# Kernel tuning notes

Hardware: AMD Instinct MI355X
Metric: run time of the kernel (lower is better)

## Reference

```python
import jax, jax.numpy as jnp
import numpy as np

B, T, S = 4, 64, 256
E_ENC = 512   # encoder_hidden_size
D_DEC = 512   # decoder_hidden_size (must equal E_ENC per original math)
F_EMB = 128   # field_embed_size


def setup_inputs() -> dict:
    key = jax.random.key(0)
    ks = jax.random.split(key, 11)
    s = 0.05
    return {
        "output": jax.random.normal(ks[0], (B, T, D_DEC), jnp.float32),
        "encoder_hidden": jax.random.normal(ks[1], (S, B, E_ENC), jnp.float32),
        "input_z": jax.random.normal(ks[2], (B, S, F_EMB), jnp.float32),
        "W1": jax.random.normal(ks[3], (D_DEC, E_ENC), jnp.float32) * s,
        "b1": jnp.zeros((D_DEC,), jnp.float32),
        "W2": jax.random.normal(ks[4], (D_DEC, D_DEC), jnp.float32) * s,
        "b2": jnp.zeros((D_DEC,), jnp.float32),
        "W3": jax.random.normal(ks[5], (D_DEC, F_EMB), jnp.float32) * s,
        "b3": jnp.zeros((D_DEC,), jnp.float32),
        "W4": jax.random.normal(ks[6], (D_DEC, D_DEC), jnp.float32) * s,
        "b4": jnp.zeros((D_DEC,), jnp.float32),
    }


def reference(output, encoder_hidden, input_z, W1, b1, W2, b2, W3, b3, W4, b4):
    # out_hs: tanh(lin1(encoder_hidden)) on [S,B,D], then .view -> reshape to [B,S,D]
    out_hs = jnp.tanh(jnp.einsum('sbe,de->sbd', encoder_hidden, W1) + b1)
    out_hs = out_hs.reshape(out_hs.shape[1], out_hs.shape[0], out_hs.shape[2])  # [B,S,D] (raw view, as in torch)
    enc_r = encoder_hidden.reshape(encoder_hidden.shape[1], encoder_hidden.shape[0], encoder_hidden.shape[2])  # [B,S,E]

    out_fds = jnp.tanh(jnp.einsum('bsf,df->bsd', input_z, W3) + b3)   # [B,S,D]
    out2 = jnp.tanh(jnp.einsum('btd,ed->bte', output, W2) + b2)       # [B,T,D]
    out3 = jnp.tanh(jnp.einsum('btd,ed->bte', output, W4) + b4)       # [B,T,D]

    # Multiplicative gates, vectorized over decoder timesteps t: [B,T,S,D]
    g1 = out_hs[:, None, :, :] * out2[:, :, None, :]
    alpha = jax.nn.softmax(g1, axis=2)   # softmax over encoder positions S
    g2 = out_fds[:, None, :, :] * out3[:, :, None, :]
    beta = jax.nn.softmax(g2, axis=2)

    q = alpha * beta
    qn = jax.lax.stop_gradient(jnp.sum(q, axis=2, keepdims=True))  # .detach() in torch
    gamma = q / qn

    attn = jnp.sum(gamma * enc_r[:, None, :, :], axis=2)           # [B,T,D]
    concat = jnp.concatenate([output, attn], axis=-1)              # [B,T,2D]
    return concat, attn
```

## Files before the change

kernel.cpp:

```cpp
#include <hip/hip_runtime.h>

#define BB 4
#define TT 64
#define SS 256
#define DD 512
#define FEMB 128

__device__ __forceinline__ float fast_tanh(float x) {
    x = fminf(fmaxf(x, -10.f), 10.f);
    float t = __expf(2.f * x);
    return (t - 1.f) / (t + 1.f);
}

__global__ __launch_bounds__(256) void gemm_tanh_kernel(
    const float* __restrict__ X, const float* __restrict__ Z, const float* __restrict__ Y,
    const float* __restrict__ W1, const float* __restrict__ b1,
    const float* __restrict__ W2, const float* __restrict__ b2,
    const float* __restrict__ W3, const float* __restrict__ b3,
    const float* __restrict__ W4, const float* __restrict__ b4,
    float* __restrict__ H, float* __restrict__ Fo,
    float* __restrict__ O2, float* __restrict__ O3)
{
    int id = blockIdx.x;
    const float* A; const float* W; const float* bias; float* C; int K;
    if (id < 128)      { A = X; W = W1; bias = b1; C = H;  K = 512; }
    else if (id < 256) { id -= 128; A = Z; W = W3; bias = b3; C = Fo; K = 128; }
    else if (id < 288) { id -= 256; A = Y; W = W2; bias = b2; C = O2; K = 512; }
    else               { id -= 288; A = Y; W = W4; bias = b4; C = O3; K = 512; }
    const int m0 = (id >> 3) * 64;
    const int n0 = (id & 7) * 64;

    __shared__ float As[16][68];
    __shared__ float Ws[16][68];

    const int tid  = threadIdx.x;
    const int lrow = tid >> 2;
    const int lkv  = tid & 3;
    const int ty   = tid >> 4;
    const int tx   = tid & 15;

    float acc[4][4] = {};

    const float* Ap = &A[(m0 + lrow) * K + lkv * 4];
    const float* Wp = &W[(n0 + lrow) * K + lkv * 4];
    float4 av = *(const float4*)Ap;
    float4 wv = *(const float4*)Wp;

    for (int k0 = 0; k0 < K; k0 += 16) {
        __syncthreads();
        As[lkv*4+0][lrow] = av.x; As[lkv*4+1][lrow] = av.y;
        As[lkv*4+2][lrow] = av.z; As[lkv*4+3][lrow] = av.w;
        Ws[lkv*4+0][lrow] = wv.x; Ws[lkv*4+1][lrow] = wv.y;
        Ws[lkv*4+2][lrow] = wv.z; Ws[lkv*4+3][lrow] = wv.w;
        __syncthreads();
        if (k0 + 16 < K) {
            av = *(const float4*)(Ap + k0 + 16);
            wv = *(const float4*)(Wp + k0 + 16);
        }
        #pragma unroll
        for (int k = 0; k < 16; ++k) {
            float4 a4 = *(const float4*)&As[k][ty * 4];
            float4 w4 = *(const float4*)&Ws[k][tx * 4];
            float a[4] = {a4.x, a4.y, a4.z, a4.w};
            float w[4] = {w4.x, w4.y, w4.z, w4.w};
            #pragma unroll
            for (int i = 0; i < 4; ++i)
                #pragma unroll
                for (int j = 0; j < 4; ++j)
                    acc[i][j] = fmaf(a[i], w[j], acc[i][j]);
        }
    }

    float4 bb = *(const float4*)&bias[n0 + tx * 4];
    float bj[4] = {bb.x, bb.y, bb.z, bb.w};
    #pragma unroll
    for (int i = 0; i < 4; ++i) {
        const int m = m0 + ty * 4 + i;
        float4 o;
        o.x = fast_tanh(acc[i][0] + bj[0]);
        o.y = fast_tanh(acc[i][1] + bj[1]);
        o.z = fast_tanh(acc[i][2] + bj[2]);
        o.w = fast_tanh(acc[i][3] + bj[3]);
        *(float4*)&C[m * DD + n0 + tx * 4] = o;
    }
}

__global__ __launch_bounds__(512) void attn_kernel(
    const float* __restrict__ H, const float* __restrict__ Fo,
    const float* __restrict__ X,
    const float* __restrict__ O2, const float* __restrict__ O3,
    const float* __restrict__ Y,
    float* __restrict__ out)
{
    const int idx = blockIdx.x;
    const int b   = (idx & 7) >> 1;
    const int rem = ((idx >> 3) << 1) | (idx & 1);
    const int t0  = (rem >> 2) * 2;
    const int dq  = rem & 3;
    const int tid = threadIdx.x;
    const int dl  = tid & 127;
    const int d   = dq * 128 + dl;
    const int sq  = tid >> 7;

    const int bt0 = b * TT + t0;
    const float u0 = O2[bt0 * DD + d],       v0 = O3[bt0 * DD + d];
    const float u1 = O2[(bt0 + 1) * DD + d], v1 = O3[(bt0 + 1) * DD + d];

    float l0 = 0.f, l1 = 0.f, a0 = 0.f, a1 = 0.f;
    const int base = (b * SS + sq * 64) * DD + d;
    const float* Hb = H  + base;
    const float* Fb = Fo + base;
    const float* Eb = X  + base;

    for (int s0 = 0; s0 < 64; s0 += 8) {
        float h[8], f[8], e[8];
        #pragma unroll
        for (int s = 0; s < 8; ++s) h[s] = Hb[(s0 + s) * DD];
        #pragma unroll
        for (int s = 0; s < 8; ++s) f[s] = Fb[(s0 + s) * DD];
        #pragma unroll
        for (int s = 0; s < 8; ++s) e[s] = Eb[(s0 + s) * DD];
        #pragma unroll
        for (int s = 0; s < 8; ++s) {
            const float w0 = fmaf(h[s], u0, f[s] * v0);
            const float x0 = __expf(w0);
            l0 += x0; a0 = fmaf(x0, e[s], a0);
            const float w1 = fmaf(h[s], u1, f[s] * v1);
            const float x1 = __expf(w1);
            l1 += x1; a1 = fmaf(x1, e[s], a1);
        }
    }

    __shared__ float red[3][128][9];
    if (sq) {
        red[sq-1][dl][0] = l0; red[sq-1][dl][1] = l1;
        red[sq-1][dl][2] = a0; red[sq-1][dl][3] = a1;
    }
    __syncthreads();
    if (sq == 0) {
        #pragma unroll
        for (int q = 0; q < 3; ++q) {
            l0 += red[q][dl][0]; l1 += red[q][dl][1];
            a0 += red[q][dl][2]; a1 += red[q][dl][3];
        }
        const float r0 = a0 / l0, r1 = a1 / l1;
        out[BB * TT * 2 * DD + bt0 * DD + d]       = r0;
        out[BB * TT * 2 * DD + (bt0 + 1) * DD + d] = r1;
        out[bt0 * 2 * DD + DD + d]                 = r0;
        out[(bt0 + 1) * 2 * DD + DD + d]           = r1;
        out[bt0 * 2 * DD + d]                      = Y[bt0 * DD + d];
        out[(bt0 + 1) * 2 * DD + d]                = Y[(bt0 + 1) * DD + d];
    }
}

extern "C" void kernel_launch(void* const* d_in, const int* in_sizes, int n_in,
                              void* d_out, int out_size, void* d_ws, size_t ws_size,
                              hipStream_t stream)
{
    const float* Y  = (const float*)d_in[0];
    const float* X  = (const float*)d_in[1];
    const float* Z  = (const float*)d_in[2];
    const float* W1 = (const float*)d_in[3];
    const float* b1 = (const float*)d_in[4];
    const float* W2 = (const float*)d_in[5];
    const float* b2 = (const float*)d_in[6];
    const float* W3 = (const float*)d_in[7];
    const float* b3 = (const float*)d_in[8];
    const float* W4 = (const float*)d_in[9];
    const float* b4 = (const float*)d_in[10];
    float* out = (float*)d_out;

    float* H  = (float*)d_ws;
    float* Fo = H  + 1024 * 512;
    float* O2 = Fo + 1024 * 512;
    float* O3 = O2 + 256 * 512;

    gemm_tanh_kernel<<<320, 256, 0, stream>>>(X, Z, Y, W1, b1, W2, b2, W3, b3, W4, b4,
                                              H, Fo, O2, O3);
    attn_kernel<<<512, 512, 0, stream>>>(H, Fo, X, O2, O3, Y, out);
}
```

Before: 118.1 us.

## Use bf16 MFMA for the four projection GEMMs with a conversion pre-pass

Adds a kernel that converts the activations and weights to bf16 in workspace. The FP32 LDS-tiled SIMT GEMM is replaced by a kernel that feeds matrix-core 16x16x32 bf16 instructions directly from global memory, with register double-buffering and no shared memory. The aim is to cut the compute time of the GEMM stage. In exchange it adds a kernel launch and extra memory traffic for the conversion, and it lowers input precision to bf16, which could push tolerance-sensitive outputs such as the exponentials in the attention kernel out of range.

```diff
diff --git a/kernel.cpp b/kernel.cpp
--- a/kernel.cpp
+++ b/kernel.cpp
@@ -6,82 +6,109 @@
 #define DD 512
 #define FEMB 128
 
+typedef __attribute__((ext_vector_type(8))) short short8;
+typedef __attribute__((ext_vector_type(4))) float floatx4;
+
 __device__ __forceinline__ float fast_tanh(float x) {
     x = fminf(fmaxf(x, -10.f), 10.f);
     float t = __expf(2.f * x);
     return (t - 1.f) / (t + 1.f);
 }
 
-__global__ __launch_bounds__(256) void gemm_tanh_kernel(
+__device__ __forceinline__ unsigned int pack_bf2(float a, float b) {
+    union { float f; unsigned int u; } ca, cb;
+    ca.f = a; cb.f = b;
+    unsigned int ua = ca.u + 0x7FFF + ((ca.u >> 16) & 1);
+    unsigned int ub = cb.u + 0x7FFF + ((cb.u >> 16) & 1);
+    return (ua >> 16) | (ub & 0xFFFF0000u);
+}
+
+__global__ __launch_bounds__(256) void cvt_kernel(
     const float* __restrict__ X, const float* __restrict__ Z, const float* __restrict__ Y,
-    const float* __restrict__ W1, const float* __restrict__ b1,
-    const float* __restrict__ W2, const float* __restrict__ b2,
-    const float* __restrict__ W3, const float* __restrict__ b3,
-    const float* __restrict__ W4, const float* __restrict__ b4,
+    const float* __restrict__ W1, const float* __restrict__ W2,
+    const float* __restrict__ W3, const float* __restrict__ W4,
+    unsigned short* __restrict__ Xb, unsigned short* __restrict__ Zb,
+    unsigned short* __restrict__ Yb, unsigned short* __restrict__ W1b,
+    unsigned short* __restrict__ W2b, unsigned short* __restrict__ W3b,
+    unsigned short* __restrict__ W4b)
+{
+    const int e = (blockIdx.x * 256 + threadIdx.x) * 4;
+    const float* src; unsigned short* dst; int off;
+    if (e < 524288)       { src = X;  dst = Xb;  off = 0; }
+    else if (e < 655360)  { src = Z;  dst = Zb;  off = 524288; }
+    else if (e < 786432)  { src = Y;  dst = Yb;  off = 655360; }
+    else if (e < 1048576) { src = W1; dst = W1b; off = 786432; }
+    else if (e < 1310720) { src = W2; dst = W2b; off = 1048576; }
+    else if (e < 1376256) { src = W3; dst = W3b; off = 1310720; }
+    else                  { src = W4; dst = W4b; off = 1376256; }
+    const int i = e - off;
+    float4 v = *(const float4*)&src[i];
+    uint2 p;
+    p.x = pack_bf2(v.x, v.y);
+    p.y = pack_bf2(v.z, v.w);
+    *(uint2*)&dst[i] = p;
+}
+
+__global__ __launch_bounds__(256) void gemm_mfma_kernel(
+    const unsigned short* __restrict__ Xb, const unsigned short* __restrict__ Zb,
+    const unsigned short* __restrict__ Yb,
+    const unsigned short* __restrict__ W1b, const unsigned short* __restrict__ W2b,
+    const unsigned short* __restrict__ W3b, const unsigned short* __restrict__ W4b,
+    const float* __restrict__ b1, const float* __restrict__ b2,
+    const float* __restrict__ b3, const float* __restrict__ b4,
     float* __restrict__ H, float* __restrict__ Fo,
     float* __restrict__ O2, float* __restrict__ O3)
 {
     int id = blockIdx.x;
-    const float* A; const float* W; const float* bias; float* C; int K;
-    if (id < 128)      { A = X; W = W1; bias = b1; C = H;  K = 512; }
-    else if (id < 256) { id -= 128; A = Z; W = W3; bias = b3; C = Fo; K = 128; }
-    else if (id < 288) { id -= 256; A = Y; W = W2; bias = b2; C = O2; K = 512; }
-    else               { id -= 288; A = Y; W = W4; bias = b4; C = O3; K = 512; }
+    const unsigned short* A; const unsigned short* W; const float* bias; float* C; int K;
+    if (id < 128)      { A = Xb; W = W1b; bias = b1; C = H;  K = 512; }
+    else if (id < 256) { id -= 128; A = Zb; W = W3b; bias = b3; C = Fo; K = 128; }
+    else if (id < 288) { id -= 256; A = Yb; W = W2b; bias = b2; C = O2; K = 512; }
+    else               { id -= 288; A = Yb; W = W4b; bias = b4; C = O3; K = 512; }
     const int m0 = (id >> 3) * 64;
     const int n0 = (id & 7) * 64;
-
-    __shared__ float As[16][68];
-    __shared__ float Ws[16][68];
-
-    const int tid  = threadIdx.x;
-    const int lrow = tid >> 2;
-    const int lkv  = tid & 3;
-    const int ty   = tid >> 4;
-    const int tx   = tid & 15;
-
-    float acc[4][4] = {};
-
-    const float* Ap = &A[(m0 + lrow) * K + lkv * 4];
-    const float* Wp = &W[(n0 + lrow) * K + lkv * 4];
-    float4 av = *(const float4*)Ap;
-    float4 wv = *(const float4*)Wp;
-
-    for (int k0 = 0; k0 < K; k0 += 16) {
-        __syncthreads();
-        As[lkv*4+0][lrow] = av.x; As[lkv*4+1][lrow] = av.y;
-        As[lkv*4+2][lrow] = av.z; As[lkv*4+3][lrow] = av.w;
-        Ws[lkv*4+0][lrow] = wv.x; Ws[lkv*4+1][lrow] = wv.y;
-        Ws[lkv*4+2][lrow] = wv.z; Ws[lkv*4+3][lrow] = wv.w;
-        __syncthreads();
-        if (k0 + 16 < K) {
-            av = *(const float4*)(Ap + k0 + 16);
-            wv = *(const float4*)(Wp + k0 + 16);
-        }
-        #pragma unroll
-        for (int k = 0; k < 16; ++k) {
-            float4 a4 = *(const float4*)&As[k][ty * 4];
-            float4 w4 = *(const float4*)&Ws[k][tx * 4];
-            float a[4] = {a4.x, a4.y, a4.z, a4.w};
-            float w[4] = {w4.x, w4.y, w4.z, w4.w};
-            #pragma unroll
-            for (int i = 0; i < 4; ++i)
-                #pragma unroll
-                for (int j = 0; j < 4; ++j)
-                    acc[i][j] = fmaf(a[i], w[j], acc[i][j]);
-        }
-    }
-
-    float4 bb = *(const float4*)&bias[n0 + tx * 4];
-    float bj[4] = {bb.x, bb.y, bb.z, bb.w};
+    const int wv   = threadIdx.x >> 6;
+    const int lane = threadIdx.x & 63;
+    const int fr   = lane & 15;
+    const int kh   = (lane >> 4) * 8;
+
+    const unsigned short* Ap = A + (m0 + wv * 16 + fr) * K + kh;
+    const unsigned short* Wp = W + (n0 + fr) * K + kh;
+    const int WS = 16 * K;
+
+    floatx4 acc0 = {0.f,0.f,0.f,0.f}, acc1 = acc0, acc2 = acc0, acc3 = acc0;
+
+    short8 a  = *(const short8*)Ap;
+    short8 w0 = *(const short8*)(Wp);
+    short8 w1 = *(const short8*)(Wp + WS);
+    short8 w2 = *(const short8*)(Wp + 2 * WS);
+    short8 w3 = *(const short8*)(Wp + 3 * WS);
+
+    for (int k0 = 0; k0 < K; k0 += 32) {
+        const int kn = (k0 + 32 < K) ? (k0 + 32) : 0;
+        short8 an  = *(const short8*)(Ap + kn);
+        short8 wn0 = *(const short8*)(Wp + kn);
+        short8 wn1 = *(const short8*)(Wp + WS + kn);
+        short8 wn2 = *(const short8*)(Wp + 2 * WS + kn);
+        short8 wn3 = *(const short8*)(Wp + 3 * WS + kn);
+        acc0 = __builtin_amdgcn_mfma_f32_16x16x32_bf16(a, w0, acc0, 0, 0, 0);
+        acc1 = __builtin_amdgcn_mfma_f32_16x16x32_bf16(a, w1, acc1, 0, 0, 0);
+        acc2 = __builtin_amdgcn_mfma_f32_16x16x32_bf16(a, w2, acc2, 0, 0, 0);
+        acc3 = __builtin_amdgcn_mfma_f32_16x16x32_bf16(a, w3, acc3, 0, 0, 0);
+        a = an; w0 = wn0; w1 = wn1; w2 = wn2; w3 = wn3;
+    }
+
+    const int orow  = m0 + wv * 16 + (lane >> 4) * 4;
+    const int ocol0 = n0 + fr;
+    const float bv0 = bias[ocol0], bv1 = bias[ocol0 + 16],
+                bv2 = bias[ocol0 + 32], bv3 = bias[ocol0 + 48];
     #pragma unroll
-    for (int i = 0; i < 4; ++i) {
-        const int m = m0 + ty * 4 + i;
-        float4 o;
-        o.x = fast_tanh(acc[i][0] + bj[0]);
-        o.y = fast_tanh(acc[i][1] + bj[1]);
-        o.z = fast_tanh(acc[i][2] + bj[2]);
-        o.w = fast_tanh(acc[i][3] + bj[3]);
-        *(float4*)&C[m * DD + n0 + tx * 4] = o;
+    for (int r = 0; r < 4; ++r) {
+        float* Cr = C + (orow + r) * DD + ocol0;
+        Cr[0]  = fast_tanh(acc0[r] + bv0);
+        Cr[16] = fast_tanh(acc1[r] + bv1);
+        Cr[32] = fast_tanh(acc2[r] + bv2);
+        Cr[48] = fast_tanh(acc3[r] + bv3);
     }
 }
 
@@ -174,8 +201,17 @@
     float* Fo = H  + 1024 * 512;
     float* O2 = Fo + 1024 * 512;
     float* O3 = O2 + 256 * 512;
-
-    gemm_tanh_kernel<<<320, 256, 0, stream>>>(X, Z, Y, W1, b1, W2, b2, W3, b3, W4, b4,
-                                              H, Fo, O2, O3);
+    unsigned short* Xb  = (unsigned short*)(O3 + 256 * 512);
+    unsigned short* Zb  = Xb  + 524288;
+    unsigned short* Yb  = Zb  + 131072;
+    unsigned short* W1b = Yb  + 131072;
+    unsigned short* W2b = W1b + 262144;
+    unsigned short* W3b = W2b + 262144;
+    unsigned short* W4b = W3b + 65536;
+
+    cvt_kernel<<<1600, 256, 0, stream>>>(X, Z, Y, W1, W2, W3, W4,
+                                         Xb, Zb, Yb, W1b, W2b, W3b, W4b);
+    gemm_mfma_kernel<<<320, 256, 0, stream>>>(Xb, Zb, Yb, W1b, W2b, W3b, W4b,
+                                              b1, b2, b3, b4, H, Fo, O2, O3);
     attn_kernel<<<512, 512, 0, stream>>>(H, Fo, X, O2, O3, Y, out);
 }
```

New measurement: 111.9 us. 1.06x faster.

## Replace FP32 shared-memory GEMM with bf16 MFMA loading operands straight from global

Applied to the files above, without the earlier changes.

The fused four-way linear+tanh GEMM now runs on MFMA 16x16x32 bf16 instructions. Each fp32 operand is truncated to bf16 with a byte permute, and fragments are loaded directly from global memory into registers with one-step prefetch, so the LDS staging and barriers are gone. This targets the scalar FMA cost of the GEMM stage. In exchange it loses precision through bf16 truncation, which feeds an exponent in the attention softmax, and it uses uncoalesced strided global loads with no LDS reuse.

```diff
diff --git a/kernel.cpp b/kernel.cpp
--- a/kernel.cpp
+++ b/kernel.cpp
@@ -6,13 +6,35 @@
 #define DD 512
 #define FEMB 128
 
+typedef __attribute__((ext_vector_type(8))) short short8;
+typedef __attribute__((ext_vector_type(4))) float floatx4;
+
 __device__ __forceinline__ float fast_tanh(float x) {
     x = fminf(fmaxf(x, -10.f), 10.f);
     float t = __expf(2.f * x);
     return (t - 1.f) / (t + 1.f);
 }
 
-__global__ __launch_bounds__(256) void gemm_tanh_kernel(
+struct f8 { float4 lo, hi; };
+__device__ __forceinline__ f8 ldf8(const float* p) {
+    f8 r;
+    r.lo = *(const float4*)p;
+    r.hi = *(const float4*)(p + 4);
+    return r;
+}
+__device__ __forceinline__ unsigned int fbits(float x) {
+    union { float f; unsigned int u; } c; c.f = x; return c.u;
+}
+__device__ __forceinline__ short8 cvt8(f8 v) {
+    union { unsigned int u[4]; short8 s; } r;
+    r.u[0] = __builtin_amdgcn_perm(fbits(v.lo.y), fbits(v.lo.x), 0x07060302u);
+    r.u[1] = __builtin_amdgcn_perm(fbits(v.lo.w), fbits(v.lo.z), 0x07060302u);
+    r.u[2] = __builtin_amdgcn_perm(fbits(v.hi.y), fbits(v.hi.x), 0x07060302u);
+    r.u[3] = __builtin_amdgcn_perm(fbits(v.hi.w), fbits(v.hi.z), 0x07060302u);
+    return r.s;
+}
+
+__global__ __launch_bounds__(256) void gemm_mfma_kernel(
     const float* __restrict__ X, const float* __restrict__ Z, const float* __restrict__ Y,
     const float* __restrict__ W1, const float* __restrict__ b1,
     const float* __restrict__ W2, const float* __restrict__ b2,
@@ -29,59 +51,53 @@
     else               { id -= 288; A = Y; W = W4; bias = b4; C = O3; K = 512; }
     const int m0 = (id >> 3) * 64;
     const int n0 = (id & 7) * 64;
+    const int wv   = threadIdx.x >> 6;
+    const int lane = threadIdx.x & 63;
+    const int fr   = lane & 15;
+    const int kh   = (lane >> 4) * 8;
 
-    __shared__ float As[16][68];
-    __shared__ float Ws[16][68];
+    const float* Ap = A + (m0 + wv * 16 + fr) * K + kh;
+    const float* Wp = W + (n0 + fr) * K + kh;
+    const int WS = 16 * K;
 
-    const int tid  = threadIdx.x;
-    const int lrow = tid >> 2;
-    const int lkv  = tid & 3;
-    const int ty   = tid >> 4;
-    const int tx   = tid & 15;
+    floatx4 acc0 = {0.f,0.f,0.f,0.f}, acc1 = acc0, acc2 = acc0, acc3 = acc0;
 
-    float acc[4][4] = {};
+    f8 ra  = ldf8(Ap);
+    f8 rw0 = ldf8(Wp);
+    f8 rw1 = ldf8(Wp + WS);
+    f8 rw2 = ldf8(Wp + 2 * WS);
+    f8 rw3 = ldf8(Wp + 3 * WS);
 
-    const float* Ap = &A[(m0 + lrow) * K + lkv * 4];
-    const float* Wp = &W[(n0 + lrow) * K + lkv * 4];
-    float4 av = *(const float4*)Ap;
-    float4 wv = *(const float4*)Wp;
-
-    for (int k0 = 0; k0 < K; k0 += 16) {
-        __syncthreads();
-        As[lkv*4+0][lrow] = av.x; As[lkv*4+1][lrow] = av.y;
-        As[lkv*4+2][lrow] = av.z; As[lkv*4+3][lrow] = av.w;
-        Ws[lkv*4+0][lrow] = wv.x; Ws[lkv*4+1][lrow] = wv.y;
-        Ws[lkv*4+2][lrow] = wv.z; Ws[lkv*4+3][lrow] = wv.w;
-        __syncthreads();
-        if (k0 + 16 < K) {
-            av = *(const float4*)(Ap + k0 + 16);
-            wv = *(const float4*)(Wp + k0 + 16);
-        }
-        #pragma unroll
-        for (int k = 0; k < 16; ++k) {
-            float4 a4 = *(const float4*)&As[k][ty * 4];
-            float4 w4 = *(const float4*)&Ws[k][tx * 4];
-            float a[4] = {a4.x, a4.y, a4.z, a4.w};
-            float w[4] = {w4.x, w4.y, w4.z, w4.w};
-            #pragma unroll
-            for (int i = 0; i < 4; ++i)
-                #pragma unroll
-                for (int j = 0; j < 4; ++j)
-                    acc[i][j] = fmaf(a[i], w[j], acc[i][j]);
-        }
+    for (int k0 = 0; k0 < K; k0 += 32) {
+        const int kn = (k0 + 32 < K) ? (k0 + 32) : 0;
+        f8 na  = ldf8(Ap + kn);
+        f8 nw0 = ldf8(Wp + kn);
+        f8 nw1 = ldf8(Wp + WS + kn);
+        f8 nw2 = ldf8(Wp + 2 * WS + kn);
+        f8 nw3 = ldf8(Wp + 3 * WS + kn);
+        short8 a  = cvt8(ra);
+        short8 w0 = cvt8(rw0);
+        short8 w1 = cvt8(rw1);
+        short8 w2 = cvt8(rw2);
+        short8 w3 = cvt8(rw3);
+        acc0 = __builtin_amdgcn_mfma_f32_16x16x32_bf16(a, w0, acc0, 0, 0, 0);
+        acc1 = __builtin_amdgcn_mfma_f32_16x16x32_bf16(a, w1, acc1, 0, 0, 0);
+        acc2 = __builtin_amdgcn_mfma_f32_16x16x32_bf16(a, w2, acc2, 0, 0, 0);
+        acc3 = __builtin_amdgcn_mfma_f32_16x16x32_bf16(a, w3, acc3, 0, 0, 0);
+        ra = na; rw0 = nw0; rw1 = nw1; rw2 = nw2; rw3 = nw3;
     }
 
-    float4 bb = *(const float4*)&bias[n0 + tx * 4];
-    float bj[4] = {bb.x, bb.y, bb.z, bb.w};
+    const int orow  = m0 + wv * 16 + (lane >> 4) * 4;
+    const int ocol0 = n0 + fr;
+    const float bv0 = bias[ocol0], bv1 = bias[ocol0 + 16],
+                bv2 = bias[ocol0 + 32], bv3 = bias[ocol0 + 48];
     #pragma unroll
-    for (int i = 0; i < 4; ++i) {
-        const int m = m0 + ty * 4 + i;
-        float4 o;
-        o.x = fast_tanh(acc[i][0] + bj[0]);
-        o.y = fast_tanh(acc[i][1] + bj[1]);
-        o.z = fast_tanh(acc[i][2] + bj[2]);
-        o.w = fast_tanh(acc[i][3] + bj[3]);
-        *(float4*)&C[m * DD + n0 + tx * 4] = o;
+    for (int r = 0; r < 4; ++r) {
+        float* Cr = C + (orow + r) * DD + ocol0;
+        Cr[0]  = fast_tanh(acc0[r] + bv0);
+        Cr[16] = fast_tanh(acc1[r] + bv1);
+        Cr[32] = fast_tanh(acc2[r] + bv2);
+        Cr[48] = fast_tanh(acc3[r] + bv3);
     }
 }
 
@@ -175,7 +191,7 @@
     float* O2 = Fo + 1024 * 512;
     float* O3 = O2 + 256 * 512;
 
-    gemm_tanh_kernel<<<320, 256, 0, stream>>>(X, Z, Y, W1, b1, W2, b2, W3, b3, W4, b4,
+    gemm_mfma_kernel<<<320, 256, 0, stream>>>(X, Z, Y, W1, b1, W2, b2, W3, b3, W4, b4,
                                               H, Fo, O2, O3);
     attn_kernel<<<512, 512, 0, stream>>>(H, Fo, X, O2, O3, Y, out);
 }
```

Result: slower. 123.1 us (+4.2%).
